# Kernel tuning notes

Measured on AMD Instinct MI355X. Metric: run time of the kernel, lower is better.

The kernel has to match this reference:

```python
import jax, jax.numpy as jnp
import numpy as np

EMBED_DIM = 128
NUM_SYMBOLS = 200000
PAD_IDX = NUM_SYMBOLS
K_NEIGHBORS = 10
PROCESS_STEPS = 4
D_MODEL = 2 * EMBED_DIM   # 256
D_INNER = 2 * D_MODEL     # 512
LSTM_HID = 2 * D_MODEL    # 512
B, F_SUP, MAX_K = 4096, 5, 64


def setup_inputs() -> dict:
    key = jax.random.key(0)
    ks = jax.random.split(key, 40)
    f = lambda i, shape, s=0.05: jax.random.normal(ks[i], shape, jnp.float32) * s
    inp = {}
    inp['query'] = jax.random.randint(ks[0], (B, 2), 0, NUM_SYMBOLS)
    inp['support'] = jax.random.randint(ks[1], (F_SUP, 2), 0, NUM_SYMBOLS)
    inp['q_l1'] = jax.random.randint(ks[2], (B, MAX_K, 2), 0, NUM_SYMBOLS + 1)
    inp['q_deg_l'] = jax.random.randint(ks[3], (B,), 0, 100)
    inp['q_r1'] = jax.random.randint(ks[4], (B, MAX_K, 2), 0, NUM_SYMBOLS + 1)
    inp['q_deg_r'] = jax.random.randint(ks[5], (B,), 0, 100)
    inp['s_l1'] = jax.random.randint(ks[6], (F_SUP, MAX_K, 2), 0, NUM_SYMBOLS + 1)
    inp['s_deg_l'] = jax.random.randint(ks[7], (F_SUP,), 0, 100)
    inp['s_r1'] = jax.random.randint(ks[8], (F_SUP, MAX_K, 2), 0, NUM_SYMBOLS + 1)
    inp['s_deg_r'] = jax.random.randint(ks[9], (F_SUP,), 0, 100)
    # learned parameters
    inp['symbol_emb'] = f(10, (NUM_SYMBOLS + 1, EMBED_DIM), 0.1).at[PAD_IDX].set(0.0)
    inp['gcn_w_w'] = f(11, (EMBED_DIM, 2 * EMBED_DIM))
    inp['gcn_w_b'] = jnp.zeros((EMBED_DIM,), jnp.float32)
    inp['gcn_b'] = jnp.zeros((EMBED_DIM,), jnp.float32)
    inp['g1_w'] = f(12, (EMBED_DIM // 2, EMBED_DIM))
    inp['g1_b'] = jnp.zeros((EMBED_DIM // 2,), jnp.float32)
    inp['ln1_g'] = jnp.ones((EMBED_DIM // 2,), jnp.float32)
    inp['ln1_b'] = jnp.zeros((EMBED_DIM // 2,), jnp.float32)
    inp['g2_w'] = f(13, (1, EMBED_DIM // 2))
    inp['g2_b'] = jnp.zeros((1,), jnp.float32)
    inp['gate_temp'] = jnp.array(1.0, jnp.float32)
    inp['se_p1_w'] = f(14, (D_INNER, D_MODEL))
    inp['se_p1_b'] = jnp.zeros((D_INNER,), jnp.float32)
    inp['se_p2_w'] = f(15, (D_MODEL, D_INNER))
    inp['se_p2_b'] = jnp.zeros((D_MODEL,), jnp.float32)
    inp['se_ln_g'] = jnp.ones((D_MODEL,), jnp.float32)
    inp['se_ln_b'] = jnp.zeros((D_MODEL,), jnp.float32)
    inp['w_ih'] = f(16, (4 * LSTM_HID, D_MODEL))
    inp['w_hh'] = f(17, (4 * LSTM_HID, LSTM_HID))
    inp['b_ih'] = jnp.zeros((4 * LSTM_HID,), jnp.float32)
    inp['b_hh'] = jnp.zeros((4 * LSTM_HID,), jnp.float32)
    return inp


def _layernorm(x, g, b, eps=1e-5):
    m = jnp.mean(x, axis=-1, keepdims=True)
    v = jnp.var(x, axis=-1, keepdims=True)
    return (x - m) / jnp.sqrt(v + eps) * g + b


def _l2norm(x):
    return x / jnp.maximum(jnp.linalg.norm(x, axis=-1, keepdims=True), 1e-12)


def _neighbor_encoder(conn, deg, self_ids, p):
    emb = p['symbol_emb']
    rel, ent = conn[:, :, 0], conn[:, :, 1]
    rel_emb = emb[rel]            # [n, K, D] gather
    ent_emb = emb[ent]            # [n, K, D]
    self_emb = emb[self_ids]      # [n, D]
    sim = jnp.einsum('nd,nkd->nk', _l2norm(self_emb), _l2norm(ent_emb))
    is_pad = (rel == PAD_IDX).astype(jnp.float32)
    sim = sim - is_pad * 1e9
    k = min(K_NEIGHBORS, conn.shape[1])
    _, k_idx = jax.lax.top_k(sim, k)
    bidx = jnp.arange(conn.shape[0])[:, None]
    k_mask = jnp.zeros(sim.shape, jnp.float32).at[bidx, k_idx].set(1.0)[..., None]
    concat = jnp.concatenate([rel_emb, ent_emb], axis=-1)   # [n, K, 2D]
    proj = jax.nn.leaky_relu(concat @ p['gcn_w_w'].T + p['gcn_w_b'] + p['gcn_b'], 0.01)
    valid = (1.0 - is_pad[..., None]) * k_mask
    denom = jnp.maximum(jnp.sum(valid, axis=1), 1.0)
    agg = jnp.sum((proj * k_mask) * valid, axis=1) / denom   # [n, D]
    h = jax.nn.relu(_layernorm(agg @ p['g1_w'].T + p['g1_b'], p['ln1_g'], p['ln1_b']))
    logit = h @ p['g2_w'].T + p['g2_b']                      # [n, 1]
    temp = jnp.clip(p['gate_temp'], 0.1, 5.0)
    gate = jax.nn.sigmoid(logit / temp) * (deg > 0).astype(jnp.float32)[:, None]
    return jnp.tanh(self_emb + gate * agg)


def _support_encoder(x, p):
    h = jax.nn.relu(x @ p['se_p1_w'].T + p['se_p1_b'])
    h = h @ p['se_p2_w'].T + p['se_p2_b']
    return _layernorm(h + x, p['se_ln_g'], p['se_ln_b'])


def _query_encoder(support, query, p):
    n = query.shape[0]
    h_r0 = jnp.zeros((n, LSTM_HID), jnp.float32)
    c0 = jnp.zeros((n, LSTM_HID), jnp.float32)

    def step(carry, _):
        h_r, c = carry
        gates = query @ p['w_ih'].T + p['b_ih'] + h_r @ p['w_hh'].T + p['b_hh']
        i, f, g, o = jnp.split(gates, 4, axis=-1)
        c = jax.nn.sigmoid(f) * c + jax.nn.sigmoid(i) * jnp.tanh(g)
        h_ = jax.nn.sigmoid(o) * jnp.tanh(c)
        h = query + h_[:, :D_MODEL]
        attn = jax.nn.softmax(h @ support.T, axis=1)
        r = attn @ support
        return (jnp.concatenate([h, r], axis=-1), c), None

    (h_r, _), _ = jax.lax.scan(step, (h_r0, c0), None, length=PROCESS_STEPS)
    return h_r[:, :D_MODEL]


def reference(query, support, q_l1, q_deg_l, q_r1, q_deg_r, s_l1, s_deg_l, s_r1, s_deg_r,
              symbol_emb, gcn_w_w, gcn_w_b, gcn_b, g1_w, g1_b, ln1_g, ln1_b, g2_w, g2_b,
              gate_temp, se_p1_w, se_p1_b, se_p2_w, se_p2_b, se_ln_g, se_ln_b,
              w_ih, w_hh, b_ih, b_hh):
    p = dict(symbol_emb=symbol_emb, gcn_w_w=gcn_w_w, gcn_w_b=gcn_w_b, gcn_b=gcn_b,
             g1_w=g1_w, g1_b=g1_b, ln1_g=ln1_g, ln1_b=ln1_b, g2_w=g2_w, g2_b=g2_b,
             gate_temp=gate_temp, se_p1_w=se_p1_w, se_p1_b=se_p1_b, se_p2_w=se_p2_w,
             se_p2_b=se_p2_b, se_ln_g=se_ln_g, se_ln_b=se_ln_b,
             w_ih=w_ih, w_hh=w_hh, b_ih=b_ih, b_hh=b_hh)
    q_left = _neighbor_encoder(q_l1, q_deg_l, query[:, 0], p)
    q_right = _neighbor_encoder(q_r1, q_deg_r, query[:, 1], p)
    query_vec = jnp.concatenate([q_left, q_right], axis=-1)      # [B, 2D]
    s_left = _neighbor_encoder(s_l1, s_deg_l, support[:, 0], p)
    s_right = _neighbor_encoder(s_r1, s_deg_r, support[:, 1], p)
    support_vec = jnp.concatenate([s_left, s_right], axis=-1)    # [F, 2D]
    support_g = jnp.mean(_support_encoder(support_vec, p), axis=0, keepdims=True)  # [1, 2D]
    query_enc = _support_encoder(query_vec, p)                   # [B, 2D]
    query_g = _query_encoder(support_g, query_enc, p)            # [B, 2D]
    return jnp.sum(query_g * support_g, axis=1)                  # [B]
```

## Files before the change

kernel.cpp:

```cpp
#include <hip/hip_runtime.h>
#include <math.h>

#define BQ 4096
#define F_SUP 5
#define MAXK 64
#define ED 128
#define DM 256
#define DI 512
#define LH 512
#define NG 2048
#define PADX 200000
#define KNB 10
#define NBTOT 8202
#define MROWS 82048
#define MREAL 82020
#define MQ 4224
#define EMB_ELEMS 25600128
#define NEMB8 3200016

typedef unsigned short u16;
typedef __attribute__((ext_vector_type(8))) short short8;
typedef __attribute__((ext_vector_type(4))) float floatx4;

__device__ __forceinline__ float sigf(float x) { return 1.0f / (1.0f + __expf(-x)); }
__device__ __forceinline__ float tanh_fast(float x) {
  float a = fabsf(x);
  float e = __expf(-2.0f * a);
  float t = (1.0f - e) / (1.0f + e);
  return copysignf(t, x);
}
__device__ __forceinline__ u16 f2bf(float f) {
  unsigned u = __float_as_uint(f);
  unsigned r = (u + 0x7FFFu + ((u >> 16) & 1u)) >> 16;
  return (u16)r;
}
__device__ __forceinline__ float bf2f(u16 u) {
  return __uint_as_float(((unsigned)u) << 16);
}
__device__ __forceinline__ void gl2lds16(const void* g, void* l) {
  __builtin_amdgcn_global_load_lds(
      (const __attribute__((address_space(1))) void*)g,
      (__attribute__((address_space(3))) void*)l, 16, 0, 0);
}

__global__ __launch_bounds__(256) void prep_all(
    const float* __restrict__ emb, u16* __restrict__ embb,
    const float* __restrict__ p1, const float* __restrict__ p2,
    const float* __restrict__ gcnw, const float* __restrict__ wih,
    const float* __restrict__ whh, const float* __restrict__ bih,
    const float* __restrict__ bhh,
    u16* __restrict__ p1b, u16* __restrict__ p2b, u16* __restrict__ gcnb,
    u16* __restrict__ wihb, u16* __restrict__ whhb, float* __restrict__ bihh,
    float* __restrict__ outz)
{
  long gid = (long)blockIdx.x * 256 + threadIdx.x;
  if (gid < (long)NEMB8) {
    long i = gid * 8;
    float4 f0 = *(const float4*)(emb + i);
    float4 f1 = *(const float4*)(emb + i + 4);
    short8 s;
    s[0]=(short)f2bf(f0.x); s[1]=(short)f2bf(f0.y); s[2]=(short)f2bf(f0.z); s[3]=(short)f2bf(f0.w);
    s[4]=(short)f2bf(f1.x); s[5]=(short)f2bf(f1.y); s[6]=(short)f2bf(f1.z); s[7]=(short)f2bf(f1.w);
    *(short8*)(embb + i) = s;
    return;
  }
  int g2 = (int)(gid - NEMB8);
  if (g2 < 131072) { p1b[g2] = f2bf(p1[g2]); }
  else if (g2 < 262144) { int i = g2 - 131072; p2b[i] = f2bf(p2[i]); }
  else if (g2 < 294912) { int i = g2 - 262144; gcnb[i] = f2bf(gcnw[i]); }
  else if (g2 < 819200) {
    int i = g2 - 294912; int p = i >> 8, k = i & 255;
    int g = (p >> 4) & 3, uu = (p >> 7) * 32 + ((p >> 6) & 1) * 16 + (p & 15);
    int n = g * 512 + uu;
    wihb[i] = f2bf(wih[(long)n * DM + k]);
  } else if (g2 < 1343488) {
    int i = g2 - 819200; int p = i >> 8, k = i & 255;
    int g = (p >> 4) & 3, uu = (p >> 7) * 32 + ((p >> 6) & 1) * 16 + (p & 15);
    int n = g * 512 + uu;
    whhb[i] = f2bf(whh[(long)n * LH + k]);
  } else if (g2 < 1345536) {
    int p = g2 - 1343488;
    int g = (p >> 4) & 3, uu = (p >> 7) * 32 + ((p >> 6) & 1) * 16 + (p & 15);
    int n = g * 512 + uu;
    bihh[p] = bih[n] + bhh[n];
  } else if (g2 < 1345536 + BQ) {
    outz[g2 - 1345536] = 0.f;
  }
}

__global__ __launch_bounds__(256) void nbr_simrank_kernel(
    const int* __restrict__ query, const int* __restrict__ support,
    const int* __restrict__ q_l1, const int* __restrict__ q_r1,
    const int* __restrict__ s_l1, const int* __restrict__ s_r1,
    const u16* __restrict__ embb, int* __restrict__ idxA, int* __restrict__ meta)
{
  __shared__ float sE[128];
  __shared__ float simS[64];
  __shared__ int relS[64], entS[64];
  int tid = threadIdx.x;
  int b = blockIdx.x;
  const int* conn; int self_id;
  if (b < BQ)              { int i = b;              conn = q_l1 + (long)i*(MAXK*2); self_id = query[2*i];   }
  else if (b < 2*BQ)       { int i = b - BQ;         conn = q_r1 + (long)i*(MAXK*2); self_id = query[2*i+1]; }
  else if (b < 2*BQ+F_SUP) { int i = b - 2*BQ;       conn = s_l1 + (long)i*(MAXK*2); self_id = support[2*i]; }
  else                     { int i = b - 2*BQ-F_SUP; conn = s_r1 + (long)i*(MAXK*2); self_id = support[2*i+1]; }

  int k = tid >> 2, part = tid & 3;
  int2 rc = *(const int2*)(conn + 2 * k);
  if (tid < 16) {
    short8 s = *(const short8*)(embb + (long)self_id * ED + tid * 8);
    #pragma unroll
    for (int j = 0; j < 8; ++j) sE[tid * 8 + j] = bf2f((u16)s[j]);
  }
  __syncthreads();

  const u16* er = embb + (long)rc.y * ED + part * 8;
  float dot = 0.f, sq = 0.f;
  #pragma unroll
  for (int i = 0; i < 4; ++i) {
    short8 e8 = *(const short8*)(er + i * 32);
    #pragma unroll
    for (int j = 0; j < 8; ++j) {
      float e = bf2f((u16)e8[j]);
      float s = sE[i * 32 + part * 8 + j];
      dot += e * s; sq += e * e;
    }
  }
  dot += __shfl_xor(dot, 1); dot += __shfl_xor(dot, 2);
  sq  += __shfl_xor(sq, 1);  sq  += __shfl_xor(sq, 2);
  if (part == 0) {
    float ne = fmaxf(sqrtf(sq), 1e-12f);
    float sim = dot / ne;
    if (rc.x == PADX) sim -= 1e9f;
    simS[k] = sim; relS[k] = rc.x; entS[k] = rc.y;
  }
  __syncthreads();

  if (tid < 64) {
    float my = simS[tid];
    int rank = 0;
    #pragma unroll
    for (int j = 0; j < 64; ++j) {
      float s = simS[j];
      rank += ((s > my) || (s == my && j < tid)) ? 1 : 0;
    }
    bool val = (rank < KNB) && (relS[tid] != PADX);
    unsigned long long vm = __ballot(val ? 1 : 0);
    int cnt = __popcll(vm);
    long base = (long)b * 10;
    if (val) {
      int pos = __popcll(vm & ((1ull << tid) - 1ull));
      int2 p; p.x = relS[tid]; p.y = entS[tid];
      *(int2*)(idxA + (base + pos) * 2) = p;
    }
    if (tid >= cnt && tid < KNB) {
      int2 pp; pp.x = PADX; pp.y = PADX;
      *(int2*)(idxA + (base + tid) * 2) = pp;
    }
    if (tid == 0) meta[b] = cnt;
  }
  if (b == 0 && tid >= 64 && tid < 64 + 2 * (MROWS - MREAL)) {
    idxA[(long)MREAL * 2 + (tid - 64)] = PADX;
  }
}

__global__ __launch_bounds__(256) void proj_gather_gemm(
    const int* __restrict__ idxA, const u16* __restrict__ embb,
    const u16* __restrict__ W, u16* __restrict__ proj)
{
// ... 116 lines not shown
    float lp = hv * g2_w[e];
    #pragma unroll
    for (int off = 1; off < 64; off <<= 1) lp += __shfl_xor(lp, off);
    if (e == 0) {
      float logit = lp + g2_b[0];
      float temp = fminf(fmaxf(gate_temp[0], 0.1f), 5.0f);
      float gate = 1.0f / (1.0f + expf(-logit / temp));
      if (deg <= 0) gate = 0.f;
      gateS = gate;
    }
  }
  __syncthreads();
  float o = tanhf(sEs[tid] + gateS * aggS[tid]);
  outp[tid] = o;
  outpb[tid] = f2bf(o);
}

__global__ __launch_bounds__(256) void gemm64(
    const u16* __restrict__ A, int lda,
    const u16* __restrict__ W, int ldw,
    int N, int K,
    float* __restrict__ Cout, u16* __restrict__ Cbf,
    const float* __restrict__ bias0, int relu)
{
  __shared__ u16 As[64 * 32];
  __shared__ u16 Bs[64 * 32];
  int tid = threadIdx.x;
  int nb = N >> 6;
  int bn = blockIdx.x % nb, bm = blockIdx.x / nb;
  int lane = tid & 63, wave = tid >> 6;
  int wm = (wave & 1) * 32, wn = (wave >> 1) * 32;
  int col = lane & 15, quad = lane >> 4;

  floatx4 acc[2][2];
  #pragma unroll
  for (int i = 0; i < 2; ++i)
    #pragma unroll
    for (int j = 0; j < 2; ++j) { floatx4 z = {0.f,0.f,0.f,0.f}; acc[i][j] = z; }

  for (int k0 = 0; k0 < K; k0 += 32) {
    {
      int r = tid >> 2, o = tid & 3;
      int og = o ^ (r & 3);
      gl2lds16(A + (long)(bm * 64 + r) * lda + k0 + og * 8, &As[(size_t)tid * 8]);
      gl2lds16(W + (long)(bn * 64 + r) * ldw + k0 + og * 8, &Bs[(size_t)tid * 8]);
    }
    __syncthreads();
    short8 af[2], bfr[2];
    #pragma unroll
    for (int i = 0; i < 2; ++i) {
      int ra = wm + i * 16 + col;
      af[i] = *(const short8*)&As[(size_t)(ra * 4 + (quad ^ (ra & 3))) * 8];
      int rb = wn + i * 16 + col;
      bfr[i] = *(const short8*)&Bs[(size_t)(rb * 4 + (quad ^ (rb & 3))) * 8];
    }
    #pragma unroll
    for (int i = 0; i < 2; ++i)
      #pragma unroll
      for (int j = 0; j < 2; ++j)
        acc[i][j] = __builtin_amdgcn_mfma_f32_16x16x32_bf16(af[i], bfr[j], acc[i][j], 0, 0, 0);
    __syncthreads();
  }

  int gm0 = bm * 64 + wm + quad * 4;
  int gn0 = bn * 64 + wn + col;
  #pragma unroll
  for (int i = 0; i < 2; ++i) {
    #pragma unroll
    for (int j = 0; j < 2; ++j) {
      int n = gn0 + j * 16;
      float bv = bias0 ? bias0[n] : 0.f;
      #pragma unroll
      for (int rr = 0; rr < 4; ++rr) {
        int m = gm0 + i * 16 + rr;
        float v = acc[i][j][rr] + bv;
        if (relu) v = fmaxf(v, 0.f);
        if (Cout) Cout[(long)m * N + n] = v;
        if (Cbf)  Cbf[(long)m * N + n] = f2bf(v);
      }
    }
  }
}

__global__ __launch_bounds__(256) void mfma_gemm(
    const u16* __restrict__ A, int lda,
    const u16* __restrict__ W, int ldw,
    int N, int K,
    const float* __restrict__ bias0,
    const u16* __restrict__ gqin,
    u16* __restrict__ gqout,
    int lstm_mode,
    float* __restrict__ cstate, const float* __restrict__ qe,
    u16* __restrict__ hbf,
    const float* __restrict__ whh_f, float* __restrict__ sgo, float* __restrict__ sco)
{
  __shared__ u16 As[128 * 32];
  __shared__ u16 Bs[128 * 32];
  int tid = threadIdx.x;

  if (lstm_mode == 2 && whh_f && blockIdx.x >= gridDim.x - 512) {
    int sc = blockIdx.x - (gridDim.x - 512);
    float* sgS = (float*)As;
    float v = 0.f;
    #pragma unroll
    for (int r = 0; r < F_SUP; ++r) v += qe[(long)(BQ + r) * DM + tid];
    v *= (1.0f / (float)F_SUP);
    sgS[tid] = v;
    if (sc == 0) sgo[tid] = v;
    __syncthreads();
    int wv = tid >> 6, lane = tid & 63;
    int n = sc * 4 + wv;
    float4 w = *(const float4*)(whh_f + (long)n * LH + DM + lane * 4);
    float4 s = *(const float4*)&sgS[lane * 4];
    float d = w.x*s.x + w.y*s.y + w.z*s.z + w.w*s.w;
    #pragma unroll
    for (int off = 1; off < 64; off <<= 1) d += __shfl_xor(d, off);
    if (lane == 0) {
      int g = n >> 9, uu = n & 511;
      int p = (uu >> 5) * 128 + ((uu >> 4) & 1) * 64 + g * 16 + (uu & 15);
      sco[p] = d;
    }
    return;
  }

  int nb = N >> 7;
  int bn = blockIdx.x % nb, bm = blockIdx.x / nb;
  int lane = tid & 63, wave = tid >> 6;
  int wm = (wave & 1) * 64, wn = (wave >> 1) * 64;
  int col = lane & 15, quad = lane >> 4;

  u16 gqa[64]; float cpv[16]; float qev[16]; float scv[4];
  int u = 0; long fb = 0;
  {
    u = bn * 32 + (wave >> 1) * 16 + col;
    fb = ((long)(bm * (NG >> 7) + bn) * 4 + wave) * 64 + lane;
    #pragma unroll
    for (int j = 0; j < 4; ++j)
      scv[j] = bias0[bn * 128 + (wave >> 1) * 64 + j * 16 + col];
    if (lstm_mode == 1) {
      const short8* gp = (const short8*)(gqin + fb * 64);
      #pragma unroll
      for (int t = 0; t < 8; ++t) *(short8*)&gqa[t * 8] = gp[t];
      const float4* cp = (const float4*)(cstate + fb * 16);
      #pragma unroll
      for (int t = 0; t < 4; ++t) *(float4*)&cpv[t * 4] = cp[t];
    }
    if (u < DM) {
      #pragma unroll
      for (int i = 0; i < 4; ++i)
        #pragma unroll
        for (int r = 0; r < 4; ++r) {
          int m = bm * 128 + (wave & 1) * 64 + i * 16 + quad * 4 + r;
          qev[i * 4 + r] = qe[(long)m * DM + u];
        }
    }
  }

  floatx4 acc[4][4];
  #pragma unroll
  for (int i = 0; i < 4; ++i)
    #pragma unroll
    for (int j = 0; j < 4; ++j) { floatx4 z = {0.f,0.f,0.f,0.f}; acc[i][j] = z; }

  for (int k0 = 0; k0 < K; k0 += 32) {
    #pragma unroll
    for (int t = 0; t < 2; ++t) {
      int c = t * 256 + tid;
      int r = c >> 2, o = c & 3;
      int og = o ^ (r & 3);
      gl2lds16(A + (long)(bm * 128 + r) * lda + k0 + og * 8, &As[(size_t)c * 8]);
      gl2lds16(W + (long)(bn * 128 + r) * ldw + k0 + og * 8, &Bs[(size_t)c * 8]);
    }
    __syncthreads();
    short8 af[4], bfr[4];
    #pragma unroll
    for (int i = 0; i < 4; ++i) {
      int ra = wm + i * 16 + col;
      af[i] = *(const short8*)&As[(size_t)(ra * 4 + (quad ^ (ra & 3))) * 8];
      int rb = wn + i * 16 + col;
      bfr[i] = *(const short8*)&Bs[(size_t)(rb * 4 + (quad ^ (rb & 3))) * 8];
    }
    #pragma unroll
    for (int i = 0; i < 4; ++i)
      #pragma unroll
      for (int j = 0; j < 4; ++j)
        acc[i][j] = __builtin_amdgcn_mfma_f32_16x16x32_bf16(af[i], bfr[j], acc[i][j], 0, 0, 0);
    __syncthreads();
  }

  {
    float cnew[16];
    #pragma unroll
    for (int i = 0; i < 4; ++i) {
      #pragma unroll
      for (int r = 0; r < 4; ++r) {
        float gI = acc[i][0][r] + scv[0];
        float gF = acc[i][1][r] + scv[1];
        float gG = acc[i][2][r] + scv[2];
        float gO = acc[i][3][r] + scv[3];
        if (lstm_mode == 1) {
          gI += bf2f(gqa[(i * 4 + 0) * 4 + r]);
          gF += bf2f(gqa[(i * 4 + 1) * 4 + r]);
          gG += bf2f(gqa[(i * 4 + 2) * 4 + r]);
          gO += bf2f(gqa[(i * 4 + 3) * 4 + r]);
        }
        float cp = (lstm_mode == 2) ? 0.f : cpv[i * 4 + r];
        float cn = sigf(gF) * cp + sigf(gI) * tanh_fast(gG);
        cnew[i * 4 + r] = cn;
        if (u < DM) {
          int m = bm * 128 + (wave & 1) * 64 + i * 16 + quad * 4 + r;
          hbf[(long)m * DM + u] = f2bf(qev[i * 4 + r] + sigf(gO) * tanh_fast(cn));
        }
      }
    }
    {
      float4* cp = (float4*)(cstate + fb * 16);
      #pragma unroll
      for (int t = 0; t < 4; ++t) cp[t] = *(float4*)&cnew[t * 4];
    }
    if (lstm_mode == 2) {
      u16 ga[64];
      #pragma unroll
      for (int i = 0; i < 4; ++i)
        #pragma unroll
        for (int j = 0; j < 4; ++j)
          #pragma unroll
          for (int r = 0; r < 4; ++r)
            ga[(i * 4 + j) * 4 + r] = f2bf(acc[i][j][r] + scv[j]);
      short8* gp = (short8*)(gqout + fb * 64);
      #pragma unroll
      for (int t = 0; t < 8; ++t) gp[t] = *(short8*)&ga[t * 8];
    }
  }
}

__global__ __launch_bounds__(256) void lstm4_dot_kernel(
    const u16* __restrict__ A,
    const u16* __restrict__ W,
    const float* __restrict__ bias0,
    const u16* __restrict__ gqin, const float* __restrict__ cstate,
    const float* __restrict__ qe, const float* __restrict__ sgv,
    float* __restrict__ dotv)
{
  __shared__ u16 As[64 * 32];
  __shared__ u16 Bs[128 * 32];
  int tid = threadIdx.x;
  int bn = blockIdx.x & 7, bm = blockIdx.x >> 3;
  int lane = tid & 63, wave = tid >> 6;
  int col = lane & 15, quad = (lane >> 4) & 3;
  int w1 = wave & 1, w2 = wave >> 1;

  int u = bn * 32 + w2 * 16 + col;
  long fb = (((long)(bm >> 1) * 16 + bn) * 4 + ((bm & 1) | (w2 << 1))) * 64 + lane;
  float scv[4], qev[8], cpv[8]; u16 gqa[32];
  #pragma unroll
  for (int j = 0; j < 4; ++j)
    scv[j] = bias0[bn * 128 + w2 * 64 + j * 16 + col];
  {
    const short8* gp = (const short8*)(gqin + fb * 64);
    const float4* cp = (const float4*)(cstate + fb * 16);
    #pragma unroll
    for (int i = 0; i < 2; ++i) {
      int io = w1 * 2 + i;
      *(short8*)&gqa[i * 16]     = gp[io * 2];
      *(short8*)&gqa[i * 16 + 8] = gp[io * 2 + 1];
      *(float4*)&cpv[i * 4]      = cp[io];
    }
    #pragma unroll
    for (int i = 0; i < 2; ++i)
      #pragma unroll
      for (int r = 0; r < 4; ++r) {
        int m = bm * 64 + w1 * 32 + i * 16 + quad * 4 + r;
        qev[i * 4 + r] = qe[(long)m * DM + u];
      }
  }
  float sgu = sgv[u];

  floatx4 acc[2][4];
  #pragma unroll
  for (int i = 0; i < 2; ++i)
    #pragma unroll
    for (int j = 0; j < 4; ++j) { floatx4 z = {0.f,0.f,0.f,0.f}; acc[i][j] = z; }

  for (int k0 = 0; k0 < 256; k0 += 32) {
    {
      int r = tid >> 2, o = tid & 3;
      int og = o ^ (r & 3);
      gl2lds16(A + (long)(bm * 64 + r) * DM + k0 + og * 8, &As[(size_t)tid * 8]);
    }
    #pragma unroll
    for (int t = 0; t < 2; ++t) {
      int c = t * 256 + tid;
      int r = c >> 2, o = c & 3;
      int og = o ^ (r & 3);
      gl2lds16(W + (long)(bn * 128 + r) * DM + k0 + og * 8, &Bs[(size_t)c * 8]);
    }
    __syncthreads();
    short8 af[2], bfr[4];
    #pragma unroll
    for (int i = 0; i < 2; ++i) {
      int ra = w1 * 32 + i * 16 + col;
      af[i] = *(const short8*)&As[(size_t)(ra * 4 + (quad ^ (ra & 3))) * 8];
    }
    #pragma unroll
    for (int j = 0; j < 4; ++j) {
      int rb = w2 * 64 + j * 16 + col;
      bfr[j] = *(const short8*)&Bs[(size_t)(rb * 4 + (quad ^ (rb & 3))) * 8];
    }
    #pragma unroll
    for (int i = 0; i < 2; ++i)
      #pragma unroll
      for (int j = 0; j < 4; ++j)
        acc[i][j] = __builtin_amdgcn_mfma_f32_16x16x32_bf16(af[i], bfr[j], acc[i][j], 0, 0, 0);
    __syncthreads();
  }

  #pragma unroll
  for (int i = 0; i < 2; ++i) {
    #pragma unroll
    for (int r = 0; r < 4; ++r) {
      float gI = acc[i][0][r] + scv[0] + bf2f(gqa[i * 16 + 0 * 4 + r]);
      float gF = acc[i][1][r] + scv[1] + bf2f(gqa[i * 16 + 1 * 4 + r]);
      float gG = acc[i][2][r] + scv[2] + bf2f(gqa[i * 16 + 2 * 4 + r]);
      float gO = acc[i][3][r] + scv[3] + bf2f(gqa[i * 16 + 3 * 4 + r]);
      float cn = sigf(gF) * cpv[i * 4 + r] + sigf(gI) * tanh_fast(gG);
      float hv = qev[i * 4 + r] + sigf(gO) * tanh_fast(cn);
      float p = hv * sgu;
      p += __shfl_xor(p, 1); p += __shfl_xor(p, 2);
      p += __shfl_xor(p, 4); p += __shfl_xor(p, 8);
      if (col == 0) {
        int m = bm * 64 + w1 * 32 + i * 16 + quad * 4 + r;
        atomicAdd(&dotv[m], p);
      }
    }
  }
}

__global__ __launch_bounds__(256) void ln_residual_kernel(
    const float* __restrict__ h2buf, const float* __restrict__ xbuf,
    const float* __restrict__ lng, const float* __restrict__ lnb,
    float* __restrict__ out, u16* __restrict__ outb)
{
  __shared__ float red[4];
  int r = blockIdx.x, tid = threadIdx.x;
  float v = h2buf[(long)r * DM + tid] + xbuf[(long)r * DM + tid];
  float s = v;
  #pragma unroll
  for (int off = 1; off < 64; off <<= 1) s += __shfl_xor(s, off);
  if ((tid & 63) == 0) red[tid >> 6] = s;
  __syncthreads();
  float mean = (red[0] + red[1] + red[2] + red[3]) * (1.0f / 256.0f);
  __syncthreads();
  float dv = v - mean;
  float s2 = dv * dv;
  #pragma unroll
  for (int off = 1; off < 64; off <<= 1) s2 += __shfl_xor(s2, off);
  if ((tid & 63) == 0) red[tid >> 6] = s2;
  __syncthreads();
  float var = (red[0] + red[1] + red[2] + red[3]) * (1.0f / 256.0f);
  float o = dv / sqrtf(var + 1e-5f) * lng[tid] + lnb[tid];
  out[(long)r * DM + tid] = o;
  outb[(long)r * DM + tid] = f2bf(o);
}

extern "C" void kernel_launch(void* const* d_in, const int* in_sizes, int n_in,
                              void* d_out, int out_size, void* d_ws, size_t ws_size,
                              hipStream_t stream)
{
  const int*   query    = (const int*)  d_in[0];
  const int*   support  = (const int*)  d_in[1];
  const int*   q_l1     = (const int*)  d_in[2];
  const int*   q_deg_l  = (const int*)  d_in[3];
  const int*   q_r1     = (const int*)  d_in[4];
  const int*   q_deg_r  = (const int*)  d_in[5];
  const int*   s_l1     = (const int*)  d_in[6];
  const int*   s_deg_l  = (const int*)  d_in[7];
  const int*   s_r1     = (const int*)  d_in[8];
  const int*   s_deg_r  = (const int*)  d_in[9];
  const float* symbol_emb = (const float*)d_in[10];
  const float* gcn_w_w  = (const float*)d_in[11];
  const float* gcn_w_b  = (const float*)d_in[12];
  const float* gcn_b    = (const float*)d_in[13];
  const float* g1_w     = (const float*)d_in[14];
  const float* g1_b     = (const float*)d_in[15];
  const float* ln1_g    = (const float*)d_in[16];
  const float* ln1_b    = (const float*)d_in[17];
  const float* g2_w     = (const float*)d_in[18];
  const float* g2_b     = (const float*)d_in[19];
  const float* gate_temp= (const float*)d_in[20];
  const float* se_p1_w  = (const float*)d_in[21];
  const float* se_p1_b  = (const float*)d_in[22];
  const float* se_p2_w  = (const float*)d_in[23];
  const float* se_p2_b  = (const float*)d_in[24];
  const float* se_ln_g  = (const float*)d_in[25];
  const float* se_ln_b  = (const float*)d_in[26];
  const float* w_ih     = (const float*)d_in[27];
  const float* w_hh     = (const float*)d_in[28];
  const float* b_ih     = (const float*)d_in[29];
  const float* b_hh     = (const float*)d_in[30];

  float* ws = (float*)d_ws;
  size_t off = 0;
  float* projF   = ws + off; off += (size_t)MROWS * 128 / 2;
  float* idxF    = ws + off; off += (size_t)MROWS * 2;
  float* qv      = ws + off; off += (size_t)MQ * DM;
  float* qe      = ws + off; off += (size_t)MQ * DM;
  float* qv_bfF  = ws + off; off += (size_t)MQ * DM / 2;
  float* qe_bfF  = ws + off; off += (size_t)MQ * DM / 2;
  float* h1bF    = ws + off; off += (size_t)MQ * DI / 2;
  float* H2      = ws + off; off += (size_t)MQ * DM;
  float* gqbF    = ws + off; off += (size_t)BQ * NG / 2;
  float* cstate  = ws + off; off += (size_t)BQ * LH;
  float* hbf0F   = ws + off; off += (size_t)BQ * DM / 2;
  float* hbf1F   = ws + off; off += (size_t)BQ * DM / 2;
  float* p1bF    = ws + off; off += 131072 / 2;
  float* p2bF    = ws + off; off += 131072 / 2;
  float* gcnbF   = ws + off; off += 32768 / 2;
  float* wihbF   = ws + off; off += 524288 / 2;
  float* whhbF   = ws + off; off += 524288 / 2;
  float* bihh    = ws + off; off += 2048;
  float* sg      = ws + off; off += 256;
  float* s_corr  = ws + off; off += 2048;
  float* metaF   = ws + off; off += 8448;
  float* embbF   = ws + off; off += (size_t)EMB_ELEMS / 2;

  u16* proj   = (u16*)projF;
  int* idxA   = (int*)idxF;
  u16* qv_bf  = (u16*)qv_bfF;
  u16* qe_bf  = (u16*)qe_bfF;
  u16* H1_bf  = (u16*)h1bF;
  u16* gq_fr  = (u16*)gqbF;
  u16* hbf0   = (u16*)hbf0F;
  u16* hbf1   = (u16*)hbf1F;
  u16* p1b    = (u16*)p1bF;
  u16* p2b    = (u16*)p2bF;
  u16* gcnb   = (u16*)gcnbF;
  u16* wihb   = (u16*)wihbF;
  u16* whhb   = (u16*)whhbF;
  int* meta   = (int*)metaF;
  u16* embb   = (u16*)embbF;

  {
    long total = (long)NEMB8 + 1345536 + BQ;
    int blocks = (int)((total + 255) / 256);
    prep_all<<<blocks, 256, 0, stream>>>(symbol_emb, embb,
        se_p1_w, se_p2_w, gcn_w_w, w_ih, w_hh, b_ih, b_hh,
        p1b, p2b, gcnb, wihb, whhb, bihh, (float*)d_out);
  }

  nbr_simrank_kernel<<<NBTOT, 256, 0, stream>>>(
      query, support, q_l1, q_r1, s_l1, s_r1, embb, idxA, meta);

  proj_gather_gemm<<<MROWS / 128, 256, 0, stream>>>(idxA, embb, gcnb, proj);

  nbr_post_kernel<<<NBTOT, 128, 0, stream>>>(
      query, support, q_deg_l, q_deg_r, s_deg_l, s_deg_r, symbol_emb,
      proj, meta, gcn_w_b, gcn_b, g1_w, g1_b, ln1_g, ln1_b, g2_w, g2_b, gate_temp,
      qv, qv_bf);

  gemm64<<<(MQ / 64) * (DI / 64), 256, 0, stream>>>(qv_bf, 256, p1b, 256, DI, 256,
      nullptr, H1_bf, se_p1_b, 1);
  gemm64<<<(MQ / 64) * (DM / 64), 256, 0, stream>>>(H1_bf, 512, p2b, 512, DM, 512,
      H2, nullptr, se_p2_b, 0);
  ln_residual_kernel<<<BQ + F_SUP, 256, 0, stream>>>(H2, qv, se_ln_g, se_ln_b, qe, qe_bf);

  mfma_gemm<<<(BQ / 128) * (NG / 128) + 512, 256, 0, stream>>>(qe_bf, 256, wihb, 256, NG, 256,
      bihh, nullptr, gq_fr, 2, cstate, qe, hbf0,
      w_hh, sg, s_corr);

  mfma_gemm<<<(BQ / 128) * (NG / 128), 256, 0, stream>>>(hbf0, 256, whhb, 256, NG, 256,
      s_corr, gq_fr, nullptr, 1, cstate, qe, hbf1,
      nullptr, nullptr, nullptr);
  mfma_gemm<<<(BQ / 128) * (NG / 128), 256, 0, stream>>>(hbf1, 256, whhb, 256, NG, 256,
      s_corr, gq_fr, nullptr, 1, cstate, qe, hbf0,
      nullptr, nullptr, nullptr);

  lstm4_dot_kernel<<<(BQ / 64) * 8, 256, 0, stream>>>(hbf0, whhb, s_corr,
      gq_fr, cstate, qe, sg, (float*)d_out);
}
```

Measured before the change: 393.4 us.

## Fuse the four LSTM step kernels into one persistent kernel with grid barriers

Replaces the three mfma_gemm launches and the lstm4_dot launch with a single persistent kernel of 512 blocks. Phases are separated by a software grid barrier built on agent-scope atomic counters, which prep_all now zeroes. Because each block keeps its tile across steps, cell state and the precomputed input-gate fragments stay in registers instead of being written and reread between steps. This removes launch gaps and some global traffic. In exchange, correctness depends on all 512 blocks being co-resident, otherwise the barrier deadlocks, and the spin barrier adds its own latency at each phase.

```diff
diff --git a/kernel.cpp b/kernel.cpp
--- a/kernel.cpp
+++ b/kernel.cpp
@@ -17,6 +17,7 @@
 #define MQ 4224
 #define EMB_ELEMS 25600128
 #define NEMB8 3200016
+#define LSTM_BLKS 512
 
 typedef unsigned short u16;
 typedef __attribute__((ext_vector_type(8))) short short8;
@@ -41,6 +42,18 @@
   __builtin_amdgcn_global_load_lds(
       (const __attribute__((address_space(1))) void*)g,
       (__attribute__((address_space(3))) void*)l, 16, 0, 0);
+}
+
+__device__ __forceinline__ void grid_sync(int* cnt) {
+  __threadfence();
+  __syncthreads();
+  if (threadIdx.x == 0) {
+    __hip_atomic_fetch_add(cnt, 1, __ATOMIC_ACQ_REL, __HIP_MEMORY_SCOPE_AGENT);
+    while (__hip_atomic_load(cnt, __ATOMIC_ACQUIRE, __HIP_MEMORY_SCOPE_AGENT) < LSTM_BLKS)
+      __builtin_amdgcn_s_sleep(8);
+  }
+  __syncthreads();
+  __threadfence();
 }
 
 __global__ __launch_bounds__(256) void prep_all(
@@ -51,7 +64,7 @@
     const float* __restrict__ bhh,
     u16* __restrict__ p1b, u16* __restrict__ p2b, u16* __restrict__ gcnb,
     u16* __restrict__ wihb, u16* __restrict__ whhb, float* __restrict__ bihh,
-    float* __restrict__ outz)
+    float* __restrict__ outz, int* __restrict__ scnt)
 {
   long gid = (long)blockIdx.x * 256 + threadIdx.x;
   if (gid < (long)NEMB8) {
@@ -85,6 +98,8 @@
     bihh[p] = bih[n] + bhh[n];
   } else if (g2 < 1345536 + BQ) {
     outz[g2 - 1345536] = 0.f;
+  } else if (g2 < 1345536 + BQ + 8) {
+    scnt[g2 - 1345536 - BQ] = 0;
   }
 }
 
@@ -367,260 +382,6 @@
   }
 }
 
-__global__ __launch_bounds__(256) void mfma_gemm(
-    const u16* __restrict__ A, int lda,
-    const u16* __restrict__ W, int ldw,
-    int N, int K,
-    const float* __restrict__ bias0,
-    const u16* __restrict__ gqin,
-    u16* __restrict__ gqout,
-    int lstm_mode,
-    float* __restrict__ cstate, const float* __restrict__ qe,
-    u16* __restrict__ hbf,
-    const float* __restrict__ whh_f, float* __restrict__ sgo, float* __restrict__ sco)
-{
-  __shared__ u16 As[128 * 32];
-  __shared__ u16 Bs[128 * 32];
-  int tid = threadIdx.x;
-
-  if (lstm_mode == 2 && whh_f && blockIdx.x >= gridDim.x - 512) {
-    int sc = blockIdx.x - (gridDim.x - 512);
-    float* sgS = (float*)As;
-    float v = 0.f;
-    #pragma unroll
-    for (int r = 0; r < F_SUP; ++r) v += qe[(long)(BQ + r) * DM + tid];
-    v *= (1.0f / (float)F_SUP);
-    sgS[tid] = v;
-    if (sc == 0) sgo[tid] = v;
-    __syncthreads();
-    int wv = tid >> 6, lane = tid & 63;
-    int n = sc * 4 + wv;
-    float4 w = *(const float4*)(whh_f + (long)n * LH + DM + lane * 4);
-    float4 s = *(const float4*)&sgS[lane * 4];
-    float d = w.x*s.x + w.y*s.y + w.z*s.z + w.w*s.w;
-    #pragma unroll
-    for (int off = 1; off < 64; off <<= 1) d += __shfl_xor(d, off);
-    if (lane == 0) {
-      int g = n >> 9, uu = n & 511;
-      int p = (uu >> 5) * 128 + ((uu >> 4) & 1) * 64 + g * 16 + (uu & 15);
-      sco[p] = d;
-    }
-    return;
-  }
-
-  int nb = N >> 7;
-  int bn = blockIdx.x % nb, bm = blockIdx.x / nb;
-  int lane = tid & 63, wave = tid >> 6;
-  int wm = (wave & 1) * 64, wn = (wave >> 1) * 64;
-  int col = lane & 15, quad = lane >> 4;
-
-  u16 gqa[64]; float cpv[16]; float qev[16]; float scv[4];
-  int u = 0; long fb = 0;
-  {
-    u = bn * 32 + (wave >> 1) * 16 + col;
-    fb = ((long)(bm * (NG >> 7) + bn) * 4 + wave) * 64 + lane;
-    #pragma unroll
-    for (int j = 0; j < 4; ++j)
-      scv[j] = bias0[bn * 128 + (wave >> 1) * 64 + j * 16 + col];
-    if (lstm_mode == 1) {
-      const short8* gp = (const short8*)(gqin + fb * 64);
-      #pragma unroll
-      for (int t = 0; t < 8; ++t) *(short8*)&gqa[t * 8] = gp[t];
-      const float4* cp = (const float4*)(cstate + fb * 16);
-      #pragma unroll
-      for (int t = 0; t < 4; ++t) *(float4*)&cpv[t * 4] = cp[t];
-    }
-    if (u < DM) {
-      #pragma unroll
-      for (int i = 0; i < 4; ++i)
-        #pragma unroll
-        for (int r = 0; r < 4; ++r) {
-          int m = bm * 128 + (wave & 1) * 64 + i * 16 + quad * 4 + r;
-          qev[i * 4 + r] = qe[(long)m * DM + u];
-        }
-    }
-  }
-
-  floatx4 acc[4][4];
-  #pragma unroll
-  for (int i = 0; i < 4; ++i)
-    #pragma unroll
-    for (int j = 0; j < 4; ++j) { floatx4 z = {0.f,0.f,0.f,0.f}; acc[i][j] = z; }
-
-  for (int k0 = 0; k0 < K; k0 += 32) {
-    #pragma unroll
-    for (int t = 0; t < 2; ++t) {
-      int c = t * 256 + tid;
-      int r = c >> 2, o = c & 3;
-      int og = o ^ (r & 3);
-      gl2lds16(A + (long)(bm * 128 + r) * lda + k0 + og * 8, &As[(size_t)c * 8]);
-      gl2lds16(W + (long)(bn * 128 + r) * ldw + k0 + og * 8, &Bs[(size_t)c * 8]);
-    }
-    __syncthreads();
-    short8 af[4], bfr[4];
-    #pragma unroll
-    for (int i = 0; i < 4; ++i) {
-      int ra = wm + i * 16 + col;
-      af[i] = *(const short8*)&As[(size_t)(ra * 4 + (quad ^ (ra & 3))) * 8];
-      int rb = wn + i * 16 + col;
-      bfr[i] = *(const short8*)&Bs[(size_t)(rb * 4 + (quad ^ (rb & 3))) * 8];
-    }
-    #pragma unroll
-    for (int i = 0; i < 4; ++i)
-      #pragma unroll
-      for (int j = 0; j < 4; ++j)
-        acc[i][j] = __builtin_amdgcn_mfma_f32_16x16x32_bf16(af[i], bfr[j], acc[i][j], 0, 0, 0);
-    __syncthreads();
-  }
-
-  {
-    float cnew[16];
-    #pragma unroll
-    for (int i = 0; i < 4; ++i) {
-      #pragma unroll
-      for (int r = 0; r < 4; ++r) {
-        float gI = acc[i][0][r] + scv[0];
-        float gF = acc[i][1][r] + scv[1];
-        float gG = acc[i][2][r] + scv[2];
-        float gO = acc[i][3][r] + scv[3];
-        if (lstm_mode == 1) {
-          gI += bf2f(gqa[(i * 4 + 0) * 4 + r]);
-          gF += bf2f(gqa[(i * 4 + 1) * 4 + r]);
-          gG += bf2f(gqa[(i * 4 + 2) * 4 + r]);
-          gO += bf2f(gqa[(i * 4 + 3) * 4 + r]);
-        }
-        float cp = (lstm_mode == 2) ? 0.f : cpv[i * 4 + r];
-        float cn = sigf(gF) * cp + sigf(gI) * tanh_fast(gG);
-        cnew[i * 4 + r] = cn;
-        if (u < DM) {
-          int m = bm * 128 + (wave & 1) * 64 + i * 16 + quad * 4 + r;
-          hbf[(long)m * DM + u] = f2bf(qev[i * 4 + r] + sigf(gO) * tanh_fast(cn));
-        }
-      }
-    }
-    {
-      float4* cp = (float4*)(cstate + fb * 16);
-      #pragma unroll
-      for (int t = 0; t < 4; ++t) cp[t] = *(float4*)&cnew[t * 4];
-    }
-    if (lstm_mode == 2) {
-      u16 ga[64];
-      #pragma unroll
-      for (int i = 0; i < 4; ++i)
-        #pragma unroll
-        for (int j = 0; j < 4; ++j)
-          #pragma unroll
-          for (int r = 0; r < 4; ++r)
-            ga[(i * 4 + j) * 4 + r] = f2bf(acc[i][j][r] + scv[j]);
-      short8* gp = (short8*)(gqout + fb * 64);
-      #pragma unroll
-      for (int t = 0; t < 8; ++t) gp[t] = *(short8*)&ga[t * 8];
-    }
-  }
-}
-
-__global__ __launch_bounds__(256) void lstm4_dot_kernel(
-    const u16* __restrict__ A,
-    const u16* __restrict__ W,
-    const float* __restrict__ bias0,
-    const u16* __restrict__ gqin, const float* __restrict__ cstate,
-    const float* __restrict__ qe, const float* __restrict__ sgv,
-    float* __restrict__ dotv)
-{
-  __shared__ u16 As[64 * 32];
-  __shared__ u16 Bs[128 * 32];
-  int tid = threadIdx.x;
-  int bn = blockIdx.x & 7, bm = blockIdx.x >> 3;
-  int lane = tid & 63, wave = tid >> 6;
-  int col = lane & 15, quad = (lane >> 4) & 3;
-  int w1 = wave & 1, w2 = wave >> 1;
-
-  int u = bn * 32 + w2 * 16 + col;
-  long fb = (((long)(bm >> 1) * 16 + bn) * 4 + ((bm & 1) | (w2 << 1))) * 64 + lane;
-  float scv[4], qev[8], cpv[8]; u16 gqa[32];
-  #pragma unroll
-  for (int j = 0; j < 4; ++j)
-    scv[j] = bias0[bn * 128 + w2 * 64 + j * 16 + col];
-  {
-    const short8* gp = (const short8*)(gqin + fb * 64);
-    const float4* cp = (const float4*)(cstate + fb * 16);
-    #pragma unroll
-    for (int i = 0; i < 2; ++i) {
-      int io = w1 * 2 + i;
-      *(short8*)&gqa[i * 16]     = gp[io * 2];
-      *(short8*)&gqa[i * 16 + 8] = gp[io * 2 + 1];
-      *(float4*)&cpv[i * 4]      = cp[io];
-    }
-    #pragma unroll
-    for (int i = 0; i < 2; ++i)
-      #pragma unroll
-      for (int r = 0; r < 4; ++r) {
-        int m = bm * 64 + w1 * 32 + i * 16 + quad * 4 + r;
-        qev[i * 4 + r] = qe[(long)m * DM + u];
-      }
-  }
-  float sgu = sgv[u];
-
-  floatx4 acc[2][4];
-  #pragma unroll
-  for (int i = 0; i < 2; ++i)
-    #pragma unroll
-    for (int j = 0; j < 4; ++j) { floatx4 z = {0.f,0.f,0.f,0.f}; acc[i][j] = z; }
-
-  for (int k0 = 0; k0 < 256; k0 += 32) {
-    {
-      int r = tid >> 2, o = tid & 3;
-      int og = o ^ (r & 3);
-      gl2lds16(A + (long)(bm * 64 + r) * DM + k0 + og * 8, &As[(size_t)tid * 8]);
-    }
-    #pragma unroll
-    for (int t = 0; t < 2; ++t) {
-      int c = t * 256 + tid;
-      int r = c >> 2, o = c & 3;
-      int og = o ^ (r & 3);
-      gl2lds16(W + (long)(bn * 128 + r) * DM + k0 + og * 8, &Bs[(size_t)c * 8]);
-    }
-    __syncthreads();
-    short8 af[2], bfr[4];
-    #pragma unroll
-    for (int i = 0; i < 2; ++i) {
-      int ra = w1 * 32 + i * 16 + col;
-      af[i] = *(const short8*)&As[(size_t)(ra * 4 + (quad ^ (ra & 3))) * 8];
-    }
-    #pragma unroll
-    for (int j = 0; j < 4; ++j) {
-      int rb = w2 * 64 + j * 16 + col;
-      bfr[j] = *(const short8*)&Bs[(size_t)(rb * 4 + (quad ^ (rb & 3))) * 8];
-    }
-    #pragma unroll
-    for (int i = 0; i < 2; ++i)
-      #pragma unroll
-      for (int j = 0; j < 4; ++j)
-        acc[i][j] = __builtin_amdgcn_mfma_f32_16x16x32_bf16(af[i], bfr[j], acc[i][j], 0, 0, 0);
-    __syncthreads();
-  }
-
-  #pragma unroll
-  for (int i = 0; i < 2; ++i) {
-    #pragma unroll
-    for (int r = 0; r < 4; ++r) {
-      float gI = acc[i][0][r] + scv[0] + bf2f(gqa[i * 16 + 0 * 4 + r]);
-      float gF = acc[i][1][r] + scv[1] + bf2f(gqa[i * 16 + 1 * 4 + r]);
-      float gG = acc[i][2][r] + scv[2] + bf2f(gqa[i * 16 + 2 * 4 + r]);
-      float gO = acc[i][3][r] + scv[3] + bf2f(gqa[i * 16 + 3 * 4 + r]);
-      float cn = sigf(gF) * cpv[i * 4 + r] + sigf(gI) * tanh_fast(gG);
-      float hv = qev[i * 4 + r] + sigf(gO) * tanh_fast(cn);
-      float p = hv * sgu;
-      p += __shfl_xor(p, 1); p += __shfl_xor(p, 2);
-      p += __shfl_xor(p, 4); p += __shfl_xor(p, 8);
-      if (col == 0) {
-        int m = bm * 64 + w1 * 32 + i * 16 + quad * 4 + r;
-        atomicAdd(&dotv[m], p);
-      }
-    }
-  }
-}
-
 __global__ __launch_bounds__(256) void ln_residual_kernel(
     const float* __restrict__ h2buf, const float* __restrict__ xbuf,
     const float* __restrict__ lng, const float* __restrict__ lnb,
@@ -646,6 +407,262 @@
   float o = dv / sqrtf(var + 1e-5f) * lng[tid] + lnb[tid];
   out[(long)r * DM + tid] = o;
   outb[(long)r * DM + tid] = f2bf(o);
+}
+
+__device__ __forceinline__ void kloop128(
+    const u16* __restrict__ A, const u16* __restrict__ W,
+    u16* As, u16* Bs, int bm, int bn, int tid,
+    int wm, int wn, int col, int quad, floatx4 (&acc)[4][4])
+{
+  for (int k0 = 0; k0 < 256; k0 += 32) {
+    #pragma unroll
+    for (int t = 0; t < 2; ++t) {
+      int c = t * 256 + tid;
+      int r = c >> 2, o = c & 3;
+      int og = o ^ (r & 3);
+      gl2lds16(A + (long)(bm * 128 + r) * 256 + k0 + og * 8, &As[(size_t)c * 8]);
+      gl2lds16(W + (long)(bn * 128 + r) * 256 + k0 + og * 8, &Bs[(size_t)c * 8]);
+    }
+    __syncthreads();
+    short8 af[4], bfr[4];
+    #pragma unroll
+    for (int i = 0; i < 4; ++i) {
+      int ra = wm + i * 16 + col;
+      af[i] = *(const short8*)&As[(size_t)(ra * 4 + (quad ^ (ra & 3))) * 8];
+      int rb = wn + i * 16 + col;
+      bfr[i] = *(const short8*)&Bs[(size_t)(rb * 4 + (quad ^ (rb & 3))) * 8];
+    }
+    #pragma unroll
+    for (int i = 0; i < 4; ++i)
+      #pragma unroll
+      for (int j = 0; j < 4; ++j)
+        acc[i][j] = __builtin_amdgcn_mfma_f32_16x16x32_bf16(af[i], bfr[j], acc[i][j], 0, 0, 0);
+    __syncthreads();
+  }
+}
+
+__global__ __launch_bounds__(256, 2) void lstm_all(
+    const u16* __restrict__ qe_bf, const u16* __restrict__ wihb,
+    const u16* __restrict__ whhb, const float* __restrict__ bihh,
+    const float* __restrict__ qe, const float* __restrict__ whh_f,
+    u16* __restrict__ gq_fr, float* __restrict__ cstate,
+    u16* __restrict__ hbf0, u16* __restrict__ hbf1,
+    float* __restrict__ sg, float* __restrict__ s_corr,
+    float* __restrict__ dotv, int* __restrict__ scnt)
+{
+  __shared__ u16 As[128 * 32];
+  __shared__ u16 Bs[128 * 32];
+  int tid = threadIdx.x;
+  int blk = blockIdx.x;
+  int lane = tid & 63, wave = tid >> 6;
+  int col = lane & 15, quad = lane >> 4;
+
+  {
+    float* sgS = (float*)As;
+    float v = 0.f;
+    #pragma unroll
+    for (int r = 0; r < F_SUP; ++r) v += qe[(long)(BQ + r) * DM + tid];
+    v *= (1.0f / (float)F_SUP);
+    sgS[tid] = v;
+    if (blk == 0) sg[tid] = v;
+    __syncthreads();
+    int n = blk * 4 + wave;
+    float4 w = *(const float4*)(whh_f + (long)n * LH + DM + lane * 4);
+    float4 s = *(const float4*)&sgS[lane * 4];
+    float d = w.x*s.x + w.y*s.y + w.z*s.z + w.w*s.w;
+    #pragma unroll
+    for (int off = 1; off < 64; off <<= 1) d += __shfl_xor(d, off);
+    if (lane == 0) {
+      int g = n >> 9, uu = n & 511;
+      int p = (uu >> 5) * 128 + ((uu >> 4) & 1) * 64 + g * 16 + (uu & 15);
+      s_corr[p] = d;
+    }
+    __syncthreads();
+  }
+
+  int bn = blk & 15, bm = blk >> 4;
+  int wm = (wave & 1) * 64, wn = (wave >> 1) * 64;
+  int u = bn * 32 + (wave >> 1) * 16 + col;
+  long fb = ((long)blk * 4 + wave) * 64 + lane;
+
+  float qev[16];
+  if (u < DM) {
+    #pragma unroll
+    for (int i = 0; i < 4; ++i)
+      #pragma unroll
+      for (int r = 0; r < 4; ++r) {
+        int m = bm * 128 + (wave & 1) * 64 + i * 16 + quad * 4 + r;
+        qev[i * 4 + r] = qe[(long)m * DM + u];
+      }
+  }
+
+  u16 gqa[64];
+  float cc[16];
+
+  {
+    float scv[4];
+    #pragma unroll
+    for (int j = 0; j < 4; ++j)
+      scv[j] = bihh[bn * 128 + (wave >> 1) * 64 + j * 16 + col];
+    floatx4 acc[4][4];
+    #pragma unroll
+    for (int i = 0; i < 4; ++i)
+      #pragma unroll
+      for (int j = 0; j < 4; ++j) { floatx4 z = {0.f,0.f,0.f,0.f}; acc[i][j] = z; }
+    kloop128(qe_bf, wihb, As, Bs, bm, bn, tid, wm, wn, col, quad, acc);
+    #pragma unroll
+    for (int i = 0; i < 4; ++i)
+      #pragma unroll
+      for (int j = 0; j < 4; ++j)
+        #pragma unroll
+        for (int r = 0; r < 4; ++r)
+          gqa[(i * 4 + j) * 4 + r] = f2bf(acc[i][j][r] + scv[j]);
+    short8* gp = (short8*)(gq_fr + fb * 64);
+    #pragma unroll
+    for (int t = 0; t < 8; ++t) gp[t] = *(short8*)&gqa[t * 8];
+    #pragma unroll
+    for (int i = 0; i < 4; ++i)
+      #pragma unroll
+      for (int r = 0; r < 4; ++r) {
+        float gI = acc[i][0][r] + scv[0];
+        float gG = acc[i][2][r] + scv[2];
+        float gO = acc[i][3][r] + scv[3];
+        float cn = sigf(gI) * tanh_fast(gG);
+        cc[i * 4 + r] = cn;
+        if (u < DM) {
+          int m = bm * 128 + (wave & 1) * 64 + i * 16 + quad * 4 + r;
+          hbf0[(long)m * DM + u] = f2bf(qev[i * 4 + r] + sigf(gO) * tanh_fast(cn));
+        }
+      }
+  }
+  grid_sync(&scnt[0]);
+
+  float scv2[4];
+  #pragma unroll
+  for (int j = 0; j < 4; ++j)
+    scv2[j] = s_corr[bn * 128 + (wave >> 1) * 64 + j * 16 + col];
+
+  #pragma unroll 1
+  for (int step = 0; step < 2; ++step) {
+    const u16* Ain = step ? hbf1 : hbf0;
+    u16* hout = step ? hbf0 : hbf1;
+    floatx4 acc[4][4];
+    #pragma unroll
+    for (int i = 0; i < 4; ++i)
+      #pragma unroll
+      for (int j = 0; j < 4; ++j) { floatx4 z = {0.f,0.f,0.f,0.f}; acc[i][j] = z; }
+    kloop128(Ain, whhb, As, Bs, bm, bn, tid, wm, wn, col, quad, acc);
+    #pragma unroll
+    for (int i = 0; i < 4; ++i)
+      #pragma unroll
+      for (int r = 0; r < 4; ++r) {
+        float gI = acc[i][0][r] + scv2[0] + bf2f(gqa[(i * 4 + 0) * 4 + r]);
+        float gF = acc[i][1][r] + scv2[1] + bf2f(gqa[(i * 4 + 1) * 4 + r]);
+        float gG = acc[i][2][r] + scv2[2] + bf2f(gqa[(i * 4 + 2) * 4 + r]);
+        float gO = acc[i][3][r] + scv2[3] + bf2f(gqa[(i * 4 + 3) * 4 + r]);
+        float cn = sigf(gF) * cc[i * 4 + r] + sigf(gI) * tanh_fast(gG);
+        cc[i * 4 + r] = cn;
+        if (u < DM) {
+          int m = bm * 128 + (wave & 1) * 64 + i * 16 + quad * 4 + r;
+          hout[(long)m * DM + u] = f2bf(qev[i * 4 + r] + sigf(gO) * tanh_fast(cn));
+        }
+      }
+    if (step == 1) {
+      float4* cp = (float4*)(cstate + fb * 16);
+      #pragma unroll
+      for (int t = 0; t < 4; ++t) cp[t] = *(float4*)&cc[t * 4];
+    }
+    grid_sync(&scnt[1 + step]);
+  }
+
+  {
+    int bn4 = blk & 7, bm4 = blk >> 3;
+    int w1 = wave & 1, w2 = wave >> 1;
+    int u4 = bn4 * 32 + w2 * 16 + col;
+    long fb4 = (((long)(bm4 >> 1) * 16 + bn4) * 4 + ((bm4 & 1) | (w2 << 1))) * 64 + lane;
+    float scv4[4], qev4[8], cpv4[8]; u16 gqa4[32];
+    #pragma unroll
+    for (int j = 0; j < 4; ++j)
+      scv4[j] = s_corr[bn4 * 128 + w2 * 64 + j * 16 + col];
+    {
+      const short8* gp = (const short8*)(gq_fr + fb4 * 64);
+      const float4* cp = (const float4*)(cstate + fb4 * 16);
+      #pragma unroll
+      for (int i = 0; i < 2; ++i) {
+        int io = w1 * 2 + i;
+        *(short8*)&gqa4[i * 16]     = gp[io * 2];
+        *(short8*)&gqa4[i * 16 + 8] = gp[io * 2 + 1];
+        *(float4*)&cpv4[i * 4]      = cp[io];
+      }
+      #pragma unroll
+      for (int i = 0; i < 2; ++i)
+        #pragma unroll
+        for (int r = 0; r < 4; ++r) {
+          int m = bm4 * 64 + w1 * 32 + i * 16 + quad * 4 + r;
+          qev4[i * 4 + r] = qe[(long)m * DM + u4];
+        }
+    }
+    float sgu = sg[u4];
+
+    floatx4 acc[2][4];
+    #pragma unroll
+    for (int i = 0; i < 2; ++i)
+      #pragma unroll
+      for (int j = 0; j < 4; ++j) { floatx4 z = {0.f,0.f,0.f,0.f}; acc[i][j] = z; }
+
+    for (int k0 = 0; k0 < 256; k0 += 32) {
+      {
+        int r = tid >> 2, o = tid & 3;
+        int og = o ^ (r & 3);
+        gl2lds16(hbf0 + (long)(bm4 * 64 + r) * DM + k0 + og * 8, &As[(size_t)tid * 8]);
+      }
+      #pragma unroll
+      for (int t = 0; t < 2; ++t) {
+        int c = t * 256 + tid;
+        int r = c >> 2, o = c & 3;
+        int og = o ^ (r & 3);
+        gl2lds16(whhb + (long)(bn4 * 128 + r) * DM + k0 + og * 8, &Bs[(size_t)c * 8]);
+      }
+      __syncthreads();
+      short8 af[2], bfr[4];
+      #pragma unroll
+      for (int i = 0; i < 2; ++i) {
+        int ra = w1 * 32 + i * 16 + col;
+        af[i] = *(const short8*)&As[(size_t)(ra * 4 + (quad ^ (ra & 3))) * 8];
+      }
+      #pragma unroll
+      for (int j = 0; j < 4; ++j) {
+        int rb = w2 * 64 + j * 16 + col;
+        bfr[j] = *(const short8*)&Bs[(size_t)(rb * 4 + (quad ^ (rb & 3))) * 8];
+      }
+      #pragma unroll
+      for (int i = 0; i < 2; ++i)
+        #pragma unroll
+        for (int j = 0; j < 4; ++j)
+          acc[i][j] = __builtin_amdgcn_mfma_f32_16x16x32_bf16(af[i], bfr[j], acc[i][j], 0, 0, 0);
+      __syncthreads();
+    }
+
+    #pragma unroll
+    for (int i = 0; i < 2; ++i) {
+      #pragma unroll
+      for (int r = 0; r < 4; ++r) {
+        float gI = acc[i][0][r] + scv4[0] + bf2f(gqa4[i * 16 + 0 * 4 + r]);
+        float gF = acc[i][1][r] + scv4[1] + bf2f(gqa4[i * 16 + 1 * 4 + r]);
+        float gG = acc[i][2][r] + scv4[2] + bf2f(gqa4[i * 16 + 2 * 4 + r]);
+        float gO = acc[i][3][r] + scv4[3] + bf2f(gqa4[i * 16 + 3 * 4 + r]);
+        float cn = sigf(gF) * cpv4[i * 4 + r] + sigf(gI) * tanh_fast(gG);
+        float hv = qev4[i * 4 + r] + sigf(gO) * tanh_fast(cn);
+        float p = hv * sgu;
+        p += __shfl_xor(p, 1); p += __shfl_xor(p, 2);
+        p += __shfl_xor(p, 4); p += __shfl_xor(p, 8);
+        if (col == 0) {
+          int m = bm4 * 64 + w1 * 32 + i * 16 + quad * 4 + r;
+          atomicAdd(&dotv[m], p);
+        }
+      }
+    }
+  }
 }
 
 extern "C" void kernel_launch(void* const* d_in, const int* in_sizes, int n_in,
@@ -707,6 +724,7 @@
   float* sg      = ws + off; off += 256;
   float* s_corr  = ws + off; off += 2048;
   float* metaF   = ws + off; off += 8448;
+  float* scntF   = ws + off; off += 8;
   float* embbF   = ws + off; off += (size_t)EMB_ELEMS / 2;
 
   u16* proj   = (u16*)projF;
@@ -723,14 +741,15 @@
   u16* wihb   = (u16*)wihbF;
   u16* whhb   = (u16*)whhbF;
   int* meta   = (int*)metaF;
+  int* scnt   = (int*)scntF;
   u16* embb   = (u16*)embbF;
 
   {
-    long total = (long)NEMB8 + 1345536 + BQ;
+    long total = (long)NEMB8 + 1345536 + BQ + 8;
     int blocks = (int)((total + 255) / 256);
     prep_all<<<blocks, 256, 0, stream>>>(symbol_emb, embb,
         se_p1_w, se_p2_w, gcn_w_w, w_ih, w_hh, b_ih, b_hh,
-        p1b, p2b, gcnb, wihb, whhb, bihh, (float*)d_out);
+        p1b, p2b, gcnb, wihb, whhb, bihh, (float*)d_out, scnt);
   }
 
   nbr_simrank_kernel<<<NBTOT, 256, 0, stream>>>(
@@ -749,17 +768,6 @@
       H2, nullptr, se_p2_b, 0);
   ln_residual_kernel<<<BQ + F_SUP, 256, 0, stream>>>(H2, qv, se_ln_g, se_ln_b, qe, qe_bf);
 
-  mfma_gemm<<<(BQ / 128) * (NG / 128) + 512, 256, 0, stream>>>(qe_bf, 256, wihb, 256, NG, 256,
-      bihh, nullptr, gq_fr, 2, cstate, qe, hbf0,
-      w_hh, sg, s_corr);
-
-  mfma_gemm<<<(BQ / 128) * (NG / 128), 256, 0, stream>>>(hbf0, 256, whhb, 256, NG, 256,
-      s_corr, gq_fr, nullptr, 1, cstate, qe, hbf1,
-      nullptr, nullptr, nullptr);
-  mfma_gemm<<<(BQ / 128) * (NG / 128), 256, 0, stream>>>(hbf1, 256, whhb, 256, NG, 256,
-      s_corr, gq_fr, nullptr, 1, cstate, qe, hbf0,
-      nullptr, nullptr, nullptr);
-
-  lstm4_dot_kernel<<<(BQ / 64) * 8, 256, 0, stream>>>(hbf0, whhb, s_corr,
-      gq_fr, cstate, qe, sg, (float*)d_out);
-}
+  lstm_all<<<LSTM_BLKS, 256, 0, stream>>>(qe_bf, wihb, whhb, bihh, qe, w_hh,
+      gq_fr, cstate, hbf0, hbf1, sg, s_corr, (float*)d_out, scnt);
+}
```

Result: slower. 913.5 us (+132.2%).
